# Kernel optimization log

Hardware: AMD Instinct MI355X
Metric: run time of the kernel (lower is better)

Reference implementation:

```python
import jax, jax.numpy as jnp
from jax import lax
import numpy as np

B, C_IN, H, W = 256, 2, 15, 15
DIM_MID, DIM_OUT = 128, 64
N_RES = 4  # DirectionalConvResBlocks

# tap positions inside a 3x3 kernel for each of the 4 line directions
# (matches DirectionalConvLayer.weight_func_map: horiz, vert, diag, anti-diag)
_POS = (((1, 0), (1, 1), (1, 2)),
        ((0, 1), (1, 1), (2, 1)),
        ((0, 0), (1, 1), (2, 2)),
        ((2, 0), (1, 1), (0, 2)))


def _dir_kernel(w3, d):
    # w3: [3, O, I] -> [O, I, 3, 3] with taps placed along direction d
    O, I = w3.shape[1], w3.shape[2]
    kern = jnp.zeros((O, I, 3, 3), w3.dtype)
    for k, (r, c) in enumerate(_POS[d]):
        kern = kern.at[:, :, r, c].set(w3[k])
    return kern


def _dconv(x, w3, b, d):
    kern = _dir_kernel(w3, d)
    y = lax.conv_general_dilated(x, kern, window_strides=(1, 1),
                                 padding=((1, 1), (1, 1)),
                                 dimension_numbers=('NCHW', 'OIHW', 'NCHW'))
    return y + b[None, :, None, None]


def _pw(x, w, b):
    # 1x1 conv: w [O, I]
    return jnp.einsum('bihw,oi->bohw', x, w) + b[None, :, None, None]


def setup_inputs() -> dict:
    key = jax.random.key(0)
    ks = jax.random.split(key, 16)
    s_in = 1.0 / np.sqrt(3 * C_IN)
    s_mid = 1.0 / np.sqrt(3 * DIM_MID)
    s_pw = 1.0 / np.sqrt(DIM_MID)
    return {
        'x': jax.random.normal(ks[0], (B, C_IN, H, W), jnp.float32),
        'dconv0_w': jax.random.normal(ks[1], (3, DIM_MID, C_IN), jnp.float32) * s_in,
        'dconv0_b': jnp.zeros((DIM_MID,), jnp.float32),
        'rb_dconv_w': jax.random.normal(ks[2], (N_RES, 3, DIM_MID, DIM_MID), jnp.float32) * s_mid,
        'rb_dconv_b': jnp.zeros((N_RES, DIM_MID), jnp.float32),
        'rb_c1_w': jax.random.normal(ks[3], (N_RES, DIM_MID, DIM_MID), jnp.float32) * s_pw,
        'rb_c1_b': jnp.zeros((N_RES, DIM_MID), jnp.float32),
        'c0_w1': jax.random.normal(ks[4], (DIM_MID, DIM_MID), jnp.float32) * s_pw,
        'c0_b1': jnp.zeros((DIM_MID,), jnp.float32),
        'c0_w2': jax.random.normal(ks[5], (DIM_MID, DIM_MID), jnp.float32) * s_pw,
        'c0_b2': jnp.zeros((DIM_MID,), jnp.float32),
        'final_w': jax.random.normal(ks[6], (DIM_OUT, DIM_MID), jnp.float32) * s_pw,
        'final_b': jnp.zeros((DIM_OUT,), jnp.float32),
    }


def reference(x, dconv0_w, dconv0_b, rb_dconv_w, rb_dconv_b, rb_c1_w, rb_c1_b,
              c0_w1, c0_b1, c0_w2, c0_b2, final_w, final_b):
    silu = jax.nn.silu
    outs = []
    for d in range(4):  # 4 board directions, shared weights
        h = silu(_dconv(x, dconv0_w, dconv0_b, d))
        for i in range(N_RES):  # DirectionalConvResBlock
            r = h
            h = silu(_dconv(h, rb_dconv_w[i], rb_dconv_b[i], d))
            h = silu(_pw(h, rb_c1_w[i], rb_c1_b[i]))
            h = h + r
        # Conv0dResBlock
        r = h
        h = silu(_pw(h, c0_w1, c0_b1))
        h = silu(_pw(h, c0_w2, c0_b2))
        h = h + r
        outs.append(_pw(h, final_w, final_b))
    return jnp.stack(outs, axis=1)  # [B, 4, DIM_OUT, H, W]
```

## Files before the change

### kernel.cpp

```cpp
#include <hip/hip_runtime.h>
#include <cstdint>
#include <cstddef>


#define HWX 15
#define NPOS 225
#define CH 128
#define CHOUT 64
#define NTH 512
#define PADG 17
#define PPN (PADG*PADG)
#define ROWB (CH*2)
#define WOFF 0
#define WBYTES (CH*CH*2)
#define HOFF WBYTES
#define LDS_BYTES (HOFF + PPN*ROWB)
#define SAFE_PP (8*PADG+8)

typedef _Float16 f16;
typedef __attribute__((ext_vector_type(8))) _Float16 f16x8;
typedef __attribute__((ext_vector_type(4))) _Float16 f16x4;
typedef __attribute__((ext_vector_type(4))) float f32x4;

__device__ __forceinline__ int haddr(int pp, int ch){
  return HOFF + pp*ROWB + ((ch*2) ^ ((pp&15)<<4));
}
__device__ __forceinline__ int waddr(int o, int i){
  return WOFF + o*256 + ((i*2) ^ ((o&15)<<4));
}
__device__ __forceinline__ float silu_f(float v){ return v / (1.f + __expf(-v)); }

template<int MT>
__device__ __forceinline__ void zacc(f32x4* a){
#pragma unroll
  for (int m=0;m<MT;m++) a[m] = (f32x4){0.f,0.f,0.f,0.f};
}

template<int MT, int KB>
__device__ __forceinline__ void gemm(const char* sm, int pp0t, int pp1t,
                                     int krow, int col, f32x4* acc0, f32x4* acc1){
#pragma unroll
  for (int kb=0; kb<KB; kb++){
    const int ch0 = kb*32 + krow*8;
    f16x8 b0 = *(const f16x8*)(sm + haddr(pp0t, ch0));
    f16x8 b1 = *(const f16x8*)(sm + haddr(pp1t, ch0));
#pragma unroll
    for (int mt=0; mt<MT; mt++){
      f16x8 a = *(const f16x8*)(sm + waddr(mt*16+col, ch0));
      acc0[mt] = __builtin_amdgcn_mfma_f32_16x16x32_f16(a, b0, acc0[mt], 0, 0, 0);
      acc1[mt] = __builtin_amdgcn_mfma_f32_16x16x32_f16(a, b1, acc1[mt], 0, 0, 0);
    }
  }
}

__device__ __forceinline__ void stage_w(char* sm, const float* __restrict__ w,
                                        int rows, int tid){
  const int base = tid*32;
  if (base < rows*CH){
    const int o = base >> 7, i0 = base & 127;
    const float* src = w + o*CH + i0;
#pragma unroll
    for (int q=0;q<4;q++){
      float4 fa = *(const float4*)(src + q*8);
      float4 fb = *(const float4*)(src + q*8 + 4);
      f16x8 hv = { (f16)fa.x,(f16)fa.y,(f16)fa.z,(f16)fa.w,
                   (f16)fb.x,(f16)fb.y,(f16)fb.z,(f16)fb.w };
      *(f16x8*)(sm + waddr(o, i0 + q*8)) = hv;
    }
  }
}

template<int MT>
__device__ __forceinline__ void snap(const char* sm, f16x4* r, int pp, int krow){
#pragma unroll
  for (int mt=0;mt<MT;mt++)
    r[mt] = *(const f16x4*)(sm + haddr(pp, mt*16 + krow*4));
}

template<int MT, bool SILU, bool RES>
__device__ __forceinline__ void wb(char* sm, const f32x4* acc,
                                   const float* __restrict__ bias,
                                   const f16x4* rsd, int pp, bool valid, int krow){
#pragma unroll
  for (int mt=0;mt<MT;mt++){
    const int ch0 = mt*16 + krow*4;
    float4 bb = *(const float4*)(bias + ch0);
    f32x4 v = acc[mt];
    v[0]+=bb.x; v[1]+=bb.y; v[2]+=bb.z; v[3]+=bb.w;
    if (SILU){
#pragma unroll
      for (int j=0;j<4;j++) v[j] = silu_f(v[j]);
    }
    if (RES){
      f16x4 r = rsd[mt];
#pragma unroll
      for (int j=0;j<4;j++) v[j] += (float)r[j];
    }
    if (valid){
      f16x4 o = { (f16)v[0],(f16)v[1],(f16)v[2],(f16)v[3] };
      *(f16x4*)(sm + haddr(pp, ch0)) = o;
    }
  }
}

struct P {
  const float *x, *w0, *b0, *wdc, *bdc, *wc1, *bc1, *w01, *b01, *w02, *b02, *wf, *bf;
};

__global__ __launch_bounds__(NTH, 1)
void mix9_mfma(const P p, float* __restrict__ out)
{
  __shared__ char sm[LDS_BYTES];
  const int tid  = threadIdx.x;
  const int lane = tid & 63;
  const int wave = tid >> 6;
  const int col  = lane & 15;
  const int krow = lane >> 4;
  const int d = blockIdx.x & 3;
  const int b = blockIdx.x >> 2;

  for (int i = tid*16; i < PPN*ROWB; i += NTH*16)
    *(f32x4*)(sm + HOFF + i) = (f32x4){0.f,0.f,0.f,0.f};
  for (int i = tid*16; i < WBYTES; i += NTH*16)
    *(f32x4*)(sm + i) = (f32x4){0.f,0.f,0.f,0.f};
  __syncthreads();

  for (int i = tid; i < 2*NPOS; i += NTH){
    const int ic = i / NPOS, n = i % NPOS;
    const int pp = (n/HWX + 1)*PADG + (n%HWX + 1);
    *(f16*)(sm + haddr(pp, ic)) = (f16)p.x[(size_t)b*2*NPOS + i];
  }

  const int nt0 = wave*2, nt1 = wave*2 + 1;
  const int n0 = nt0*16 + col, n1 = nt1*16 + col;
  const bool v0 = n0 < NPOS, v1 = n1 < NPOS;
  const int pp0 = v0 ? (n0/HWX + 1)*PADG + (n0%HWX + 1) : SAFE_PP;
  const int pp1 = v1 ? (n1/HWX + 1)*PADG + (n1%HWX + 1) : SAFE_PP;

  int dneg;
  switch (d){
    case 0:  dneg = -1;        break;
    case 1:  dneg = -PADG;     break;
    case 2:  dneg = -PADG - 1; break;
    default: dneg =  PADG - 1; break;
  }
  const int tap[3] = { dneg, 0, -dneg };

  f32x4 acc0[8], acc1[8];
  f16x4 rsd0[8], rsd1[8];
  __syncthreads();

  zacc<8>(acc0); zacc<8>(acc1);
#pragma unroll 1
  for (int k=0;k<3;k++){
    if (tid < 256)
      *(f16*)(sm + waddr(tid>>1, tid&1)) = (f16)p.w0[k*256 + tid];
    __syncthreads();
    gemm<8,1>(sm, pp0+tap[k], pp1+tap[k], krow, col, acc0, acc1);
    __syncthreads();
  }
  wb<8,true,false>(sm, acc0, p.b0, nullptr, pp0, v0, krow);
  wb<8,true,false>(sm, acc1, p.b0, nullptr, pp1, v1, krow);

#pragma unroll 1
  for (int res=0; res<4; res++){
    const float* wd = p.wdc + (size_t)res*3*CH*CH;
    zacc<8>(acc0); zacc<8>(acc1);
#pragma unroll 1
    for (int k=0;k<3;k++){
      stage_w(sm, wd + (size_t)k*CH*CH, CH, tid);
      __syncthreads();
      gemm<8,4>(sm, pp0+tap[k], pp1+tap[k], krow, col, acc0, acc1);
      __syncthreads();
    }
    snap<8>(sm, rsd0, pp0, krow);
    snap<8>(sm, rsd1, pp1, krow);
    wb<8,true,false>(sm, acc0, p.bdc + res*CH, nullptr, pp0, v0, krow);
    wb<8,true,false>(sm, acc1, p.bdc + res*CH, nullptr, pp1, v1, krow);

    stage_w(sm, p.wc1 + (size_t)res*CH*CH, CH, tid);
    __syncthreads();
    zacc<8>(acc0); zacc<8>(acc1);
    gemm<8,4>(sm, pp0, pp1, krow, col, acc0, acc1);
    __syncthreads();
    wb<8,true,true>(sm, acc0, p.bc1 + res*CH, rsd0, pp0, v0, krow);
    wb<8,true,true>(sm, acc1, p.bc1 + res*CH, rsd1, pp1, v1, krow);
  }

  stage_w(sm, p.w01, CH, tid);
  __syncthreads();
  zacc<8>(acc0); zacc<8>(acc1);
  gemm<8,4>(sm, pp0, pp1, krow, col, acc0, acc1);
  __syncthreads();
  snap<8>(sm, rsd0, pp0, krow);
  snap<8>(sm, rsd1, pp1, krow);
  wb<8,true,false>(sm, acc0, p.b01, nullptr, pp0, v0, krow);
  wb<8,true,false>(sm, acc1, p.b01, nullptr, pp1, v1, krow);

  stage_w(sm, p.w02, CH, tid);
  __syncthreads();
  zacc<8>(acc0); zacc<8>(acc1);
  gemm<8,4>(sm, pp0, pp1, krow, col, acc0, acc1);
  __syncthreads();
  wb<8,true,true>(sm, acc0, p.b02, rsd0, pp0, v0, krow);
  wb<8,true,true>(sm, acc1, p.b02, rsd1, pp1, v1, krow);

  stage_w(sm, p.wf, CHOUT, tid);
  __syncthreads();
  zacc<4>(acc0); zacc<4>(acc1);
  gemm<4,4>(sm, pp0, pp1, krow, col, acc0, acc1);

  float* ob = out + ((size_t)(b*4 + d)*CHOUT)*NPOS;
#pragma unroll
  for (int mt=0;mt<4;mt++){
    const int ch0 = mt*16 + krow*4;
    float4 bb = *(const float4*)(p.bf + ch0);
    const float bj[4] = {bb.x, bb.y, bb.z, bb.w};
#pragma unroll
    for (int j=0;j<4;j++){
      if (v0) ob[(size_t)(ch0+j)*NPOS + n0] = acc0[mt][j] + bj[j];
      if (v1) ob[(size_t)(ch0+j)*NPOS + n1] = acc1[mt][j] + bj[j];
    }
  }
}

extern "C" void kernel_launch(void* const* d_in, const int* in_sizes, int n_in,
                              void* d_out, int out_size, void* d_ws, size_t ws_size,
                              hipStream_t stream)
{
  (void)in_sizes; (void)n_in; (void)d_ws; (void)ws_size; (void)out_size;
  P p;
  p.x   = (const float*)d_in[0];
  p.w0  = (const float*)d_in[1];
  p.b0  = (const float*)d_in[2];
  p.wdc = (const float*)d_in[3];
  p.bdc = (const float*)d_in[4];
  p.wc1 = (const float*)d_in[5];
  p.bc1 = (const float*)d_in[6];
  p.w01 = (const float*)d_in[7];
  p.b01 = (const float*)d_in[8];
  p.w02 = (const float*)d_in[9];
  p.b02 = (const float*)d_in[10];
  p.wf  = (const float*)d_in[11];
  p.bf  = (const float*)d_in[12];

  mix9_mfma<<<dim3(256*4), dim3(NTH), 0, stream>>>(p, (float*)d_out);
}
```

Before: 533.9 us.

## Shrink LDS footprint with K-sliced weight staging and 16-wide padded grid

Weights are now staged into shared memory 32 input channels at a time (a 128x32 slice) instead of the full 128x128 matrix, and the padded activation grid switches from a 17-wide to a 16-wide row layout where each 16-lane column group maps to one image row. Together these shrink shared memory per block so launch bounds can request four blocks per CU instead of one. The cost is many more barriers and smaller, more frequent global weight loads per GEMM, plus a lane wasted per row.

```diff
diff --git a/kernel.cpp b/kernel.cpp
--- a/kernel.cpp
+++ b/kernel.cpp
@@ -6,29 +6,67 @@
 #define HWX 15
 #define NPOS 225
 #define CH 128
-#define CHOUT 64
 #define NTH 512
-#define PADG 17
-#define PPN (PADG*PADG)
-#define ROWB (CH*2)
-#define WOFF 0
-#define WBYTES (CH*CH*2)
-#define HOFF WBYTES
-#define LDS_BYTES (HOFF + PPN*ROWB)
-#define SAFE_PP (8*PADG+8)
+#define AROWB 80
+#define ABYTES (CH*AROWB)
+#define HOFF2 ABYTES
+#define GRID_SLOTS 273
+#define LDS_BYTES (ABYTES + GRID_SLOTS*256)
+#define SAFE_PP 136
 
 typedef _Float16 f16;
 typedef __attribute__((ext_vector_type(8))) _Float16 f16x8;
 typedef __attribute__((ext_vector_type(4))) _Float16 f16x4;
 typedef __attribute__((ext_vector_type(4))) float f32x4;
 
-__device__ __forceinline__ int haddr(int pp, int ch){
-  return HOFF + pp*ROWB + ((ch*2) ^ ((pp&15)<<4));
-}
-__device__ __forceinline__ int waddr(int o, int i){
-  return WOFF + o*256 + ((i*2) ^ ((o&15)<<4));
+__device__ __forceinline__ int hb_addr(int pp, int k){
+  return HOFF2 + pp*256 + ((k*2) ^ ((pp&15)<<4));
+}
+__device__ __forceinline__ int a_addr(int o, int k){
+  return o*AROWB + k*2;
 }
 __device__ __forceinline__ float silu_f(float v){ return v / (1.f + __expf(-v)); }
+
+__device__ __forceinline__ void stage_a(char* sm, const float* __restrict__ src,
+                                        int srcStride, int rows, int tid){
+  const int o = tid >> 2, kq = tid & 3;
+  if (o < rows){
+    const float* s = src + (size_t)o*srcStride + kq*8;
+    float4 fa = *(const float4*)(s);
+    float4 fb = *(const float4*)(s + 4);
+    f16x8 hv = { (f16)fa.x,(f16)fa.y,(f16)fa.z,(f16)fa.w,
+                 (f16)fb.x,(f16)fb.y,(f16)fb.z,(f16)fb.w };
+    *(f16x8*)(sm + a_addr(o, kq*8)) = hv;
+  }
+}
+
+template<int MT>
+__device__ __forceinline__ void gemm32(const char* sm, int pb0, int pb1, int ks,
+                                       int krow, int col, f32x4* acc0, f32x4* acc1){
+  const int k8 = krow*8;
+  f16x8 b0 = *(const f16x8*)(sm + hb_addr(pb0, ks + k8));
+  f16x8 b1 = *(const f16x8*)(sm + hb_addr(pb1, ks + k8));
+#pragma unroll
+  for (int mt=0; mt<MT; mt++){
+    f16x8 a = *(const f16x8*)(sm + a_addr(mt*16+col, k8));
+    acc0[mt] = __builtin_amdgcn_mfma_f32_16x16x32_f16(a, b0, acc0[mt], 0, 0, 0);
+    acc1[mt] = __builtin_amdgcn_mfma_f32_16x16x32_f16(a, b1, acc1[mt], 0, 0, 0);
+  }
+}
+
+template<int MT>
+__device__ __forceinline__ void pw_pass(char* sm, const float* __restrict__ w,
+                                        int rows, int pb0, int pb1,
+                                        int krow, int col, int tid,
+                                        f32x4* acc0, f32x4* acc1){
+#pragma unroll 1
+  for (int ks=0; ks<CH; ks+=32){
+    __syncthreads();
+    stage_a(sm, w + ks, CH, rows, tid);
+    __syncthreads();
+    gemm32<MT>(sm, pb0, pb1, ks, krow, col, acc0, acc1);
+  }
+}
 
 template<int MT>
 __device__ __forceinline__ void zacc(f32x4* a){
@@ -36,45 +74,10 @@
   for (int m=0;m<MT;m++) a[m] = (f32x4){0.f,0.f,0.f,0.f};
 }
 
-template<int MT, int KB>
-__device__ __forceinline__ void gemm(const char* sm, int pp0t, int pp1t,
-                                     int krow, int col, f32x4* acc0, f32x4* acc1){
-#pragma unroll
-  for (int kb=0; kb<KB; kb++){
-    const int ch0 = kb*32 + krow*8;
-    f16x8 b0 = *(const f16x8*)(sm + haddr(pp0t, ch0));
-    f16x8 b1 = *(const f16x8*)(sm + haddr(pp1t, ch0));
-#pragma unroll
-    for (int mt=0; mt<MT; mt++){
-      f16x8 a = *(const f16x8*)(sm + waddr(mt*16+col, ch0));
-      acc0[mt] = __builtin_amdgcn_mfma_f32_16x16x32_f16(a, b0, acc0[mt], 0, 0, 0);
-      acc1[mt] = __builtin_amdgcn_mfma_f32_16x16x32_f16(a, b1, acc1[mt], 0, 0, 0);
-    }
-  }
-}
-
-__device__ __forceinline__ void stage_w(char* sm, const float* __restrict__ w,
-                                        int rows, int tid){
-  const int base = tid*32;
-  if (base < rows*CH){
-    const int o = base >> 7, i0 = base & 127;
-    const float* src = w + o*CH + i0;
-#pragma unroll
-    for (int q=0;q<4;q++){
-      float4 fa = *(const float4*)(src + q*8);
-      float4 fb = *(const float4*)(src + q*8 + 4);
-      f16x8 hv = { (f16)fa.x,(f16)fa.y,(f16)fa.z,(f16)fa.w,
-                   (f16)fb.x,(f16)fb.y,(f16)fb.z,(f16)fb.w };
-      *(f16x8*)(sm + waddr(o, i0 + q*8)) = hv;
-    }
-  }
-}
-
-template<int MT>
-__device__ __forceinline__ void snap(const char* sm, f16x4* r, int pp, int krow){
-#pragma unroll
-  for (int mt=0;mt<MT;mt++)
-    r[mt] = *(const f16x4*)(sm + haddr(pp, mt*16 + krow*4));
+__device__ __forceinline__ void snap8(const char* sm, f16x4* r, int pp, int krow){
+#pragma unroll
+  for (int mt=0;mt<8;mt++)
+    r[mt] = *(const f16x4*)(sm + hb_addr(pp, mt*16 + krow*4));
 }
 
 template<int MT, bool SILU, bool RES>
@@ -98,7 +101,7 @@
     }
     if (valid){
       f16x4 o = { (f16)v[0],(f16)v[1],(f16)v[2],(f16)v[3] };
-      *(f16x4*)(sm + haddr(pp, ch0)) = o;
+      *(f16x4*)(sm + hb_addr(pp, ch0)) = o;
     }
   }
 }
@@ -107,8 +110,8 @@
   const float *x, *w0, *b0, *wdc, *bdc, *wc1, *bc1, *w01, *b01, *w02, *b02, *wf, *bf;
 };
 
-__global__ __launch_bounds__(NTH, 1)
-void mix9_mfma(const P p, float* __restrict__ out)
+__global__ __launch_bounds__(NTH, 4)
+void mix9_mfma2(const P p, float* __restrict__ out)
 {
   __shared__ char sm[LDS_BYTES];
   const int tid  = threadIdx.x;
@@ -119,48 +122,46 @@
   const int d = blockIdx.x & 3;
   const int b = blockIdx.x >> 2;
 
-  for (int i = tid*16; i < PPN*ROWB; i += NTH*16)
-    *(f32x4*)(sm + HOFF + i) = (f32x4){0.f,0.f,0.f,0.f};
-  for (int i = tid*16; i < WBYTES; i += NTH*16)
-    *(f32x4*)(sm + i) = (f32x4){0.f,0.f,0.f,0.f};
+  for (int i = tid; i < LDS_BYTES/16; i += NTH)
+    ((f32x4*)sm)[i] = (f32x4){0.f,0.f,0.f,0.f};
   __syncthreads();
 
   for (int i = tid; i < 2*NPOS; i += NTH){
     const int ic = i / NPOS, n = i % NPOS;
-    const int pp = (n/HWX + 1)*PADG + (n%HWX + 1);
-    *(f16*)(sm + haddr(pp, ic)) = (f16)p.x[(size_t)b*2*NPOS + i];
-  }
-
-  const int nt0 = wave*2, nt1 = wave*2 + 1;
-  const int n0 = nt0*16 + col, n1 = nt1*16 + col;
-  const bool v0 = n0 < NPOS, v1 = n1 < NPOS;
-  const int pp0 = v0 ? (n0/HWX + 1)*PADG + (n0%HWX + 1) : SAFE_PP;
-  const int pp1 = v1 ? (n1/HWX + 1)*PADG + (n1%HWX + 1) : SAFE_PP;
+    const int pp = (n/HWX + 1)*16 + (n%HWX + 1);
+    *(f16*)(sm + hb_addr(pp, ic)) = (f16)p.x[(size_t)b*2*NPOS + i];
+  }
+
+  const int r0 = wave*2, r1 = wave*2 + 1;
+  const bool v0 = (col >= 1);
+  const bool v1 = (col >= 1) && (r1 < HWX);
+  const int pb0 = v0 ? (r0+1)*16 + col : SAFE_PP;
+  const int pb1 = v1 ? (r1+1)*16 + col : SAFE_PP;
 
   int dneg;
   switch (d){
-    case 0:  dneg = -1;        break;
-    case 1:  dneg = -PADG;     break;
-    case 2:  dneg = -PADG - 1; break;
-    default: dneg =  PADG - 1; break;
+    case 0:  dneg = -1;  break;
+    case 1:  dneg = -16; break;
+    case 2:  dneg = -17; break;
+    default: dneg =  15; break;
   }
   const int tap[3] = { dneg, 0, -dneg };
 
   f32x4 acc0[8], acc1[8];
   f16x4 rsd0[8], rsd1[8];
-  __syncthreads();
 
   zacc<8>(acc0); zacc<8>(acc1);
 #pragma unroll 1
   for (int k=0;k<3;k++){
+    __syncthreads();
     if (tid < 256)
-      *(f16*)(sm + waddr(tid>>1, tid&1)) = (f16)p.w0[k*256 + tid];
-    __syncthreads();
-    gemm<8,1>(sm, pp0+tap[k], pp1+tap[k], krow, col, acc0, acc1);
-    __syncthreads();
-  }
-  wb<8,true,false>(sm, acc0, p.b0, nullptr, pp0, v0, krow);
-  wb<8,true,false>(sm, acc1, p.b0, nullptr, pp1, v1, krow);
+      *(f16*)(sm + a_addr(tid>>1, tid&1)) = (f16)p.w0[k*256 + tid];
+    __syncthreads();
+    gemm32<8>(sm, pb0+tap[k], pb1+tap[k], 0, krow, col, acc0, acc1);
+  }
+  __syncthreads();
+  wb<8,true,false>(sm, acc0, p.b0, nullptr, pb0, v0, krow);
+  wb<8,true,false>(sm, acc1, p.b0, nullptr, pb1, v1, krow);
 
 #pragma unroll 1
   for (int res=0; res<4; res++){
@@ -168,49 +169,47 @@
     zacc<8>(acc0); zacc<8>(acc1);
 #pragma unroll 1
     for (int k=0;k<3;k++){
-      stage_w(sm, wd + (size_t)k*CH*CH, CH, tid);
-      __syncthreads();
-      gemm<8,4>(sm, pp0+tap[k], pp1+tap[k], krow, col, acc0, acc1);
-      __syncthreads();
-    }
-    snap<8>(sm, rsd0, pp0, krow);
-    snap<8>(sm, rsd1, pp1, krow);
-    wb<8,true,false>(sm, acc0, p.bdc + res*CH, nullptr, pp0, v0, krow);
-    wb<8,true,false>(sm, acc1, p.bdc + res*CH, nullptr, pp1, v1, krow);
-
-    stage_w(sm, p.wc1 + (size_t)res*CH*CH, CH, tid);
-    __syncthreads();
+#pragma unroll 1
+      for (int ks=0; ks<CH; ks+=32){
+        __syncthreads();
+        stage_a(sm, wd + (size_t)k*CH*CH + ks, CH, CH, tid);
+        __syncthreads();
+        gemm32<8>(sm, pb0+tap[k], pb1+tap[k], ks, krow, col, acc0, acc1);
+      }
+    }
+    __syncthreads();
+    snap8(sm, rsd0, pb0, krow);
+    snap8(sm, rsd1, pb1, krow);
+    wb<8,true,false>(sm, acc0, p.bdc + res*CH, nullptr, pb0, v0, krow);
+    wb<8,true,false>(sm, acc1, p.bdc + res*CH, nullptr, pb1, v1, krow);
+
     zacc<8>(acc0); zacc<8>(acc1);
-    gemm<8,4>(sm, pp0, pp1, krow, col, acc0, acc1);
-    __syncthreads();
-    wb<8,true,true>(sm, acc0, p.bc1 + res*CH, rsd0, pp0, v0, krow);
-    wb<8,true,true>(sm, acc1, p.bc1 + res*CH, rsd1, pp1, v1, krow);
-  }
-
-  stage_w(sm, p.w01, CH, tid);
-  __syncthreads();
+    pw_pass<8>(sm, p.wc1 + (size_t)res*CH*CH, CH, pb0, pb1, krow, col, tid, acc0, acc1);
+    __syncthreads();
+    wb<8,true,true>(sm, acc0, p.bc1 + res*CH, rsd0, pb0, v0, krow);
+    wb<8,true,true>(sm, acc1, p.bc1 + res*CH, rsd1, pb1, v1, krow);
+  }
+
   zacc<8>(acc0); zacc<8>(acc1);
-  gemm<8,4>(sm, pp0, pp1, krow, col, acc0, acc1);
-  __syncthreads();
-  snap<8>(sm, rsd0, pp0, krow);
-  snap<8>(sm, rsd1, pp1, krow);
-  wb<8,true,false>(sm, acc0, p.b01, nullptr, pp0, v0, krow);
-  wb<8,true,false>(sm, acc1, p.b01, nullptr, pp1, v1, krow);
-
-  stage_w(sm, p.w02, CH, tid);
-  __syncthreads();
+  pw_pass<8>(sm, p.w01, CH, pb0, pb1, krow, col, tid, acc0, acc1);
+  __syncthreads();
+  snap8(sm, rsd0, pb0, krow);
+  snap8(sm, rsd1, pb1, krow);
+  wb<8,true,false>(sm, acc0, p.b01, nullptr, pb0, v0, krow);
+  wb<8,true,false>(sm, acc1, p.b01, nullptr, pb1, v1, krow);
+
   zacc<8>(acc0); zacc<8>(acc1);
-  gemm<8,4>(sm, pp0, pp1, krow, col, acc0, acc1);
-  __syncthreads();
-  wb<8,true,true>(sm, acc0, p.b02, rsd0, pp0, v0, krow);
-  wb<8,true,true>(sm, acc1, p.b02, rsd1, pp1, v1, krow);
-
-  stage_w(sm, p.wf, CHOUT, tid);
-  __syncthreads();
+  pw_pass<8>(sm, p.w02, CH, pb0, pb1, krow, col, tid, acc0, acc1);
+  __syncthreads();
+  wb<8,true,true>(sm, acc0, p.b02, rsd0, pb0, v0, krow);
+  wb<8,true,true>(sm, acc1, p.b02, rsd1, pb1, v1, krow);
+
   zacc<4>(acc0); zacc<4>(acc1);
-  gemm<4,4>(sm, pp0, pp1, krow, col, acc0, acc1);
-
-  float* ob = out + ((size_t)(b*4 + d)*CHOUT)*NPOS;
+  pw_pass<4>(sm, p.wf, 64, pb0, pb1, krow, col, tid, acc0, acc1);
+
+  float* ob = out + ((size_t)(b*4 + d)*64)*NPOS;
+  const int nb0 = r0*HWX + (col-1);
+  const int nb1 = r1*HWX + (col-1);
 #pragma unroll
   for (int mt=0;mt<4;mt++){
     const int ch0 = mt*16 + krow*4;
@@ -218,8 +217,8 @@
     const float bj[4] = {bb.x, bb.y, bb.z, bb.w};
 #pragma unroll
     for (int j=0;j<4;j++){
-      if (v0) ob[(size_t)(ch0+j)*NPOS + n0] = acc0[mt][j] + bj[j];
-      if (v1) ob[(size_t)(ch0+j)*NPOS + n1] = acc1[mt][j] + bj[j];
+      if (v0) ob[(size_t)(ch0+j)*NPOS + nb0] = acc0[mt][j] + bj[j];
+      if (v1) ob[(size_t)(ch0+j)*NPOS + nb1] = acc1[mt][j] + bj[j];
     }
   }
 }
@@ -244,5 +243,5 @@
   p.wf  = (const float*)d_in[11];
   p.bf  = (const float*)d_in[12];
 
-  mix9_mfma<<<dim3(256*4), dim3(NTH), 0, stream>>>(p, (float*)d_out);
-}
+  mix9_mfma2<<<dim3(256*4), dim3(NTH), 0, stream>>>(p, (float*)d_out);
+}
```

Result: slower. 595.1 us (+11.5%).
